# Optimization experiments

Measured on AMD Instinct MI355X. Metric: run time of the kernel, lower is better.

The kernel has to match this reference:

```python
import jax, jax.numpy as jnp
import numpy as np

B, S, D = 4, 2048, 1024
E = 8            # num_experts
H = 2 * D        # int(4*D*(1/top_k)) with top_k=2, scaling_factor='auto'


def setup_inputs() -> dict:
    key = jax.random.key(0)
    ks = jax.random.split(key, 8)
    sd = 1.0 / np.sqrt(D)
    sh = 1.0 / np.sqrt(H)
    return {
        "x": jax.random.normal(ks[0], (B, S, D), dtype=jnp.float32),
        "top_k": 2,
        "Wg": jax.random.uniform(ks[1], (D, E), jnp.float32, -sd, sd),
        "bg": jax.random.uniform(ks[2], (E,), jnp.float32, -sd, sd),
        "W1": jax.random.uniform(ks[3], (E, D, H), jnp.float32, -sd, sd),
        "b1": jax.random.uniform(ks[4], (E, H), jnp.float32, -sd, sd),
        "W2": jax.random.uniform(ks[5], (E, H, D), jnp.float32, -sh, sh),
        "b2": jax.random.uniform(ks[6], (E, D), jnp.float32, -sh, sh),
    }


def reference(x, top_k, Wg, bg, W1, b1, W2, b2):
    b, s, d = x.shape
    e = W1.shape[0]
    T = b * s
    xt = x.reshape(T, d)                                   # [T, D]
    gate_logits = xt @ Wg + bg                             # [T, E]
    gate_probas = jax.nn.softmax(gate_logits, axis=-1)
    topk_p, topk_i = jax.lax.top_k(gate_probas, top_k)     # [T, K]
    topk_p = topk_p / jnp.sum(topk_p, axis=-1, keepdims=True)
    # combine weights per expert: zero for unselected experts
    w = jnp.zeros((T, e), dtype=x.dtype).at[jnp.arange(T)[:, None], topk_i].add(topk_p)  # [T, E]
    # dense grouped FFN over experts; unselected experts are zero-weighted,
    # so the weighted combine matches the original gather-MLP-scatter math
    h = jax.nn.gelu(jnp.einsum('td,edh->teh', xt, W1) + b1, approximate=True)  # [T, E, H]
    y = jnp.einsum('teh,ehd->ted', h, W2) + b2             # [T, E, D]
    out = jnp.einsum('te,ted->td', w, y)                   # [T, D]
    return out.reshape(b, s, d)
```

## Files before the change

### kernel.cpp

```cpp
#include <hip/hip_runtime.h>

typedef unsigned short u16;
typedef short v8s __attribute__((ext_vector_type(8)));
typedef float v4f __attribute__((ext_vector_type(4)));
typedef u16 u16x8 __attribute__((ext_vector_type(8)));
typedef u16 u16x4 __attribute__((ext_vector_type(4)));

constexpr int Tn = 8192;
constexpr int Dd = 1024;
constexpr int Hh = 2048;
constexpr int Ee = 8;
constexpr int MAXP = 17;
constexpr int G1GEMM = 8 * 16 * MAXP;
constexpr int G1XTRA = 1024;

static __device__ __forceinline__ u16 f2bf(float v) {
  unsigned u = __float_as_uint(v);
  unsigned r = (u + 0x7fffu + ((u >> 16) & 1u)) >> 16;
  return (u16)r;
}

static __device__ __forceinline__ float bf2f(u16 v) {
  return __uint_as_float(((unsigned)v) << 16);
}

static __device__ __forceinline__ void gload_lds16(const u16* g, u16* l) {
  __builtin_amdgcn_global_load_lds(
      (const __attribute__((address_space(1))) unsigned int*)g,
      (__attribute__((address_space(3))) unsigned int*)l, 16, 0, 0);
}


static __device__ __forceinline__ void transpose_tile64(
    const float* __restrict__ ip, u16* __restrict__ op,
    int R, int C, int r0, int c0, bool permute, float (*tile)[65]) {
  int tid = threadIdx.x;
#pragma unroll
  for (int k = 0; k < 4; ++k) {
    int f = k * 256 + tid;
    int r = f >> 4, c4 = (f & 15) * 4;
    float4 v = *reinterpret_cast<const float4*>(ip + (size_t)(r0 + r) * C + c0 + c4);
    tile[r][c4] = v.x; tile[r][c4 + 1] = v.y; tile[r][c4 + 2] = v.z; tile[r][c4 + 3] = v.w;
  }
  __syncthreads();
  int j = tid & 7;
#pragma unroll
  for (int rr = 0; rr < 2; ++rr) {
    int oc = (tid >> 3) + rr * 32;
    u16x8 o;
    if (!permute) {
#pragma unroll
      for (int q = 0; q < 8; ++q) o[q] = f2bf(tile[j * 8 + q][oc]);
    } else {
#pragma unroll
      for (int q = 0; q < 8; ++q) {
        int p_ = j * 8 + q;
        int src = (p_ & 3) * 16 + (p_ >> 2);
        o[q] = f2bf(tile[src][oc]);
      }
    }
    *reinterpret_cast<u16x8*>(op + (size_t)(c0 + oc) * R + r0 + j * 8) = o;
  }
}

__global__ __launch_bounds__(256) void prep_kernel(
    const float* __restrict__ x, const float* __restrict__ Wg, const float* __restrict__ bg,
    int* __restrict__ topki, float* __restrict__ topkw, u16* __restrict__ xb,
    const float* __restrict__ W1, u16* __restrict__ w1t) {
  __shared__ float tile[64][65];
  int blk = blockIdx.x;

  if (blk < 4096) {
    int e = blk >> 9;
    int t = blk & 511;
    int cx = t & 31, cy = t >> 5;
    const float* ip = W1 + (size_t)e * Dd * Hh;
    u16* op = w1t + (size_t)e * Dd * Hh;
    transpose_tile64(ip, op, Dd, Hh, cy * 64, cx * 64, false, tile);
    return;
  }

  int lane = threadIdx.x & 63;
  int t = (blk - 4096) * 4 + (threadIdx.x >> 6);
  const float4* xr = reinterpret_cast<const float4*>(x + (size_t)t * Dd);
  float acc[8] = {0.f, 0.f, 0.f, 0.f, 0.f, 0.f, 0.f, 0.f};
#pragma unroll
  for (int it = 0; it < 4; ++it) {
    float4 xv = xr[it * 64 + lane];
    int r = it * 256 + lane * 4;
    ushort4 o;
    o.x = f2bf(xv.x); o.y = f2bf(xv.y); o.z = f2bf(xv.z); o.w = f2bf(xv.w);
    *reinterpret_cast<ushort4*>(xb + (size_t)t * Dd + r) = o;
    const float4* wr = reinterpret_cast<const float4*>(Wg + (size_t)r * 8);
    float xs[4] = {xv.x, xv.y, xv.z, xv.w};
#pragma unroll
    for (int q = 0; q < 4; ++q) {
      float4 a = wr[q * 2], b = wr[q * 2 + 1];
      acc[0] += xs[q] * a.x; acc[1] += xs[q] * a.y; acc[2] += xs[q] * a.z; acc[3] += xs[q] * a.w;
      acc[4] += xs[q] * b.x; acc[5] += xs[q] * b.y; acc[6] += xs[q] * b.z; acc[7] += xs[q] * b.w;
    }
  }
#pragma unroll
  for (int e = 0; e < 8; ++e) {
#pragma unroll
    for (int off = 32; off > 0; off >>= 1) acc[e] += __shfl_xor(acc[e], off, 64);
  }
  if (lane == 0) {
    float l[8];
    float mx = -1e30f;
#pragma unroll
    for (int e = 0; e < 8; ++e) { l[e] = acc[e] + bg[e]; mx = fmaxf(mx, l[e]); }
    int i0 = 0;
#pragma unroll
    for (int e = 1; e < 8; ++e) if (l[e] > l[i0]) i0 = e;
    int i1 = (i0 == 0) ? 1 : 0;
#pragma unroll
    for (int e = 0; e < 8; ++e) if (e != i0 && l[e] > l[i1]) i1 = e;
    float e0 = __expf(l[i0] - mx), e1 = __expf(l[i1] - mx);
    float inv = 1.0f / (e0 + e1);
    topki[2 * t] = i0; topki[2 * t + 1] = i1;
    topkw[2 * t] = e0 * inv; topkw[2 * t + 1] = e1 * inv;
  }
}

__global__ __launch_bounds__(512) void sort_kernel(
    const int* __restrict__ topki,
    int* __restrict__ offs, int* __restrict__ rows,
    int* __restrict__ panelE, int* __restrict__ panelB, int* __restrict__ nPanels) {
  __shared__ int scan[8][512];
  __shared__ int tot_l[8];
  __shared__ int offs_l[9];
  const int tt = threadIdx.x;
  const int base = tt * 32;

  int ev[32];
  int cnt[8] = {0, 0, 0, 0, 0, 0, 0, 0};
#pragma unroll
  for (int jj = 0; jj < 32; ++jj) {
    int e = topki[base + jj];
    ev[jj] = e;
#pragma unroll
    for (int q = 0; q < 8; ++q) cnt[q] += (e == q) ? 1 : 0;
  }
#pragma unroll
  for (int q = 0; q < 8; ++q) scan[q][tt] = cnt[q];
  __syncthreads();

  {
    int w = tt >> 6, l = tt & 63;
    int v[8];
    int s = 0;
#pragma unroll
    for (int jj = 0; jj < 8; ++jj) { v[jj] = scan[w][l * 8 + jj]; s += v[jj]; }
    int si = s;
#pragma unroll
    for (int off = 1; off < 64; off <<= 1) {
      int o = __shfl_up(si, off, 64);
      if (l >= off) si += o;
    }
    int run = si - s;
#pragma unroll
    for (int jj = 0; jj < 8; ++jj) { scan[w][l * 8 + jj] = run; run += v[jj]; }
    if (l == 63) tot_l[w] = si;
  }
  __syncthreads();

  if (tt == 0) {
    int o = 0;
#pragma unroll
    for (int e = 0; e < 8; ++e) { offs_l[e] = o; o += tot_l[e]; }
    offs_l[8] = o;
#pragma unroll
    for (int e = 0; e < 9; ++e) offs[e] = offs_l[e];
    int np = 0;
    for (int e = 0; e < 8; ++e) {
      for (int m0 = 0; m0 < tot_l[e]; m0 += 128) {
        panelE[np] = e;
        panelB[np] = offs_l[e] + m0;
        ++np;
      }
    }
    *nPanels = np;
  }
  __syncthreads();

#pragma unroll
  for (int jj = 0; jj < 32; ++jj) {
    int e = ev[jj];
    int idx = base + jj;
    int slot = scan[e][tt]++ + offs_l[e];
    rows[slot] = idx;
  }
}


__global__ __launch_bounds__(256, 2) void gemm1_kernel(
    const u16* __restrict__ xb, const u16* __restrict__ w1t, const float* __restrict__ b1,
    const int* __restrict__ offs, const int* __restrict__ rows,
    const int* __restrict__ panelE, const int* __restrict__ panelB,
    const int* __restrict__ nPanels, u16* __restrict__ hbuf,
    const float* __restrict__ W2, u16* __restrict__ w2t) {
  __shared__ __align__(16) u16 smem[2 * 128 * 64];
  u16* As = smem;
  u16* Bs = smem + 128 * 64;

  const int bid = blockIdx.x;
  if (bid >= G1GEMM) {
    float (*tile)[65] = reinterpret_cast<float (*)[65]>(smem);
    int tb = bid - G1GEMM;
#pragma unroll 1
    for (int s = 0; s < 4; ++s) {
      int tileid = tb * 4 + s;
      int e = tileid >> 9;
      int t = tileid & 511;
      int cx = t & 15, cy = t >> 4;
      if (s) __syncthreads();
      transpose_tile64(W2 + (size_t)e * Dd * Hh, w2t + (size_t)e * Dd * Hh,
                       Hh, Dd, cy * 64, cx * 64, true, tile);
    }
    return;
  }

  const int xcd = bid & 7;
  const int q = bid >> 3;
  const int n = q & 15;
  const int pi = (q >> 4) * 8 + xcd;
  if (pi >= *nPanels) return;
  const int e = panelE[pi];
  const int sbase = panelB[pi];
  const int lim = offs[e + 1];
  const int n0 = n * 128;

  const int tid = threadIdx.x;
  const int lane = tid & 63;
  const int wid = tid >> 6;
  const int wm = (wid >> 1) * 64;
  const int wn = (wid & 1) * 64;
  const int l16 = lane & 15;
  const int quad = lane >> 4;
  const int swz8 = (l16 & 7) * 8;

  const u16* aga[4];
  const u16* bga[4];
  u16* alds[4];
  u16* blds[4];
  const int lr = lane >> 3;
  const int g = (lane & 7) ^ (lr & 7);
  const int kcol = g * 8;
#pragma unroll
  for (int j = 0; j < 4; ++j) {
    int chunk = wid * 4 + j;
    int rowl = chunk * 8 + lr;
    int slot = sbase + rowl;
    if (slot >= lim) slot = sbase;
    aga[j] = xb + (size_t)(rows[slot] >> 1) * Dd + kcol;
    bga[j] = w1t + ((size_t)e * Hh + n0 + rowl) * Dd + kcol;
    alds[j] = As + chunk * 512;
    blds[j] = Bs + chunk * 512;
  }

  v4f acc[4][4];
#pragma unroll
  for (int i = 0; i < 4; ++i)
#pragma unroll
    for (int j = 0; j < 4; ++j) acc[i][j] = {0.f, 0.f, 0.f, 0.f};

  int rowAoff[4], rowBoff[4];
#pragma unroll
  for (int t_ = 0; t_ < 4; ++t_) {
    rowAoff[t_] = (wm + t_ * 16 + l16) * 64;
    rowBoff[t_] = (wn + t_ * 16 + l16) * 64;
  }

  for (int k0 = 0; k0 < Dd; k0 += 64) {
    __syncthreads();
#pragma unroll
    for (int j = 0; j < 4; ++j) gload_lds16(aga[j] + k0, alds[j]);
#pragma unroll
    for (int j = 0; j < 4; ++j) gload_lds16(bga[j] + k0, blds[j]);
    __syncthreads();

#pragma unroll
    for (int s = 0; s < 2; ++s) {
      int coff = ((s * 4 + quad) * 8) ^ swz8;
      v8s a[4], b[4];
#pragma unroll
      for (int mt = 0; mt < 4; ++mt)
        a[mt] = *reinterpret_cast<const v8s*>(&As[rowAoff[mt] + coff]);
#pragma unroll
      for (int nt = 0; nt < 4; ++nt)
        b[nt] = *reinterpret_cast<const v8s*>(&Bs[rowBoff[nt] + coff]);
#pragma unroll
      for (int mt = 0; mt < 4; ++mt)
#pragma unroll
        for (int nt = 0; nt < 4; ++nt)
          acc[mt][nt] = __builtin_amdgcn_mfma_f32_16x16x32_bf16(a[mt], b[nt], acc[mt][nt], 0, 0, 0);
    }
  }

  float b1v[4];
  const int ngbase = n0 + wn;
#pragma unroll
  for (int nt = 0; nt < 4; ++nt) b1v[nt] = b1[(size_t)e * Hh + ngbase + nt * 16 + l16];
#pragma unroll
  for (int mt = 0; mt < 4; ++mt) {
#pragma unroll
    for (int i = 0; i < 4; ++i) {
      int m = wm + mt * 16 + quad * 4 + i;
      if (sbase + m < lim) {
        u16x4 o;
#pragma unroll
        for (int nt = 0; nt < 4; ++nt) {
          float v = acc[mt][nt][i] + b1v[nt];
          float s = 1.0f / (1.0f + __expf(-1.5957691216057308f * (v + 0.044715f * v * v * v)));
          o[nt] = f2bf(v * s);
        }
        *reinterpret_cast<u16x4*>(hbuf + (size_t)(sbase + m) * Hh + ngbase + l16 * 4) = o;
      }
    }
  }
}

__global__ __launch_bounds__(256, 2) void gemm2_kernel(
    const u16* __restrict__ hbuf, const u16* __restrict__ w2t, const float* __restrict__ b2,
    const int* __restrict__ offs, const int* __restrict__ rows,
    const int* __restrict__ panelE, const int* __restrict__ panelB,
    const int* __restrict__ nPanels, u16* __restrict__ ybuf) {
  const int bid = blockIdx.x;
  const int xcd = bid & 7;
  const int q = bid >> 3;
  const int n = q & 7;
  const int pi = (q >> 3) * 8 + xcd;
  if (pi >= *nPanels) return;
  const int e = panelE[pi];
  const int sbase = panelB[pi];
  const int lim = offs[e + 1];
  const int n0 = n * 128;

  __shared__ __align__(16) u16 smem[2 * 128 * 64];
  u16* As = smem;
  u16* Bs = smem + 128 * 64;

  const int tid = threadIdx.x;
  const int lane = tid & 63;
  const int wid = tid >> 6;
  const int wm = (wid >> 1) * 64;
  const int wn = (wid & 1) * 64;
  const int l16 = lane & 15;
  const int quad = lane >> 4;
  const int swz8 = (l16 & 7) * 8;

  const u16* aga[4];
  const u16* bga[4];
  u16* alds[4];
  u16* blds[4];
  const int lr = lane >> 3;
  const int g = (lane & 7) ^ (lr & 7);
  const int kcol = g * 8;
#pragma unroll
  for (int j = 0; j < 4; ++j) {
    int chunk = wid * 4 + j;
    int rowl = chunk * 8 + lr;
    int slot = sbase + rowl;
    if (slot >= lim) slot = sbase;
    aga[j] = hbuf + (size_t)slot * Hh + kcol;
    bga[j] = w2t + ((size_t)e * Dd + n0 + rowl) * Hh + kcol;
    alds[j] = As + chunk * 512;
    blds[j] = Bs + chunk * 512;
  }

  v4f acc[4][4];
#pragma unroll
  for (int i = 0; i < 4; ++i)
#pragma unroll
    for (int j = 0; j < 4; ++j) acc[i][j] = {0.f, 0.f, 0.f, 0.f};

  int rowAoff[4], rowBoff[4];
#pragma unroll
  for (int t_ = 0; t_ < 4; ++t_) {
    rowAoff[t_] = (wm + t_ * 16 + l16) * 64;
    rowBoff[t_] = (wn + t_ * 16 + l16) * 64;
  }

  for (int k0 = 0; k0 < Hh; k0 += 64) {
    __syncthreads();
#pragma unroll
    for (int j = 0; j < 4; ++j) gload_lds16(aga[j] + k0, alds[j]);
#pragma unroll
    for (int j = 0; j < 4; ++j) gload_lds16(bga[j] + k0, blds[j]);
    __syncthreads();

#pragma unroll
    for (int s = 0; s < 2; ++s) {
      int coff = ((s * 4 + quad) * 8) ^ swz8;
      v8s a[4], b[4];
#pragma unroll
      for (int mt = 0; mt < 4; ++mt)
        a[mt] = *reinterpret_cast<const v8s*>(&As[rowAoff[mt] + coff]);
#pragma unroll
      for (int nt = 0; nt < 4; ++nt)
        b[nt] = *reinterpret_cast<const v8s*>(&Bs[rowBoff[nt] + coff]);
#pragma unroll
      for (int mt = 0; mt < 4; ++mt)
#pragma unroll
        for (int nt = 0; nt < 4; ++nt)
          acc[mt][nt] = __builtin_amdgcn_mfma_f32_16x16x32_bf16(a[mt], b[nt], acc[mt][nt], 0, 0, 0);
    }
  }

  float b2v[4];
  int ng[4];
#pragma unroll
  for (int nt = 0; nt < 4; ++nt) {
    ng[nt] = n0 + wn + nt * 16 + l16;
    b2v[nt] = b2[(size_t)e * Dd + ng[nt]];
  }
#pragma unroll
  for (int mt = 0; mt < 4; ++mt) {
#pragma unroll
    for (int i = 0; i < 4; ++i) {
      int m = wm + mt * 16 + quad * 4 + i;
      if (sbase + m < lim) {
        size_t rowbase = (size_t)rows[sbase + m] * Dd;
#pragma unroll
        for (int nt = 0; nt < 4; ++nt)
          ybuf[rowbase + ng[nt]] = f2bf(acc[mt][nt][i] + b2v[nt]);
      }
    }
  }
}

__global__ __launch_bounds__(256) void combine_kernel(
    const u16* __restrict__ ybuf, const float* __restrict__ topkw,
    float* __restrict__ out) {
  int idx = blockIdx.x * 256 + threadIdx.x;
  int t = idx >> 7;
  int d0 = (idx & 127) * 8;
  float w0 = topkw[2 * t], w1 = topkw[2 * t + 1];
  uint4 ya = *reinterpret_cast<const uint4*>(ybuf + (size_t)(2 * t) * Dd + d0);
  uint4 yb = *reinterpret_cast<const uint4*>(ybuf + (size_t)(2 * t + 1) * Dd + d0);
  float r[8];
  const unsigned* pa = &ya.x;
  const unsigned* pb = &yb.x;
#pragma unroll
  for (int j = 0; j < 4; ++j) {
    unsigned a = pa[j], b = pb[j];
    r[2 * j]     = w0 * bf2f((u16)(a & 0xffff)) + w1 * bf2f((u16)(b & 0xffff));
    r[2 * j + 1] = w0 * bf2f((u16)(a >> 16))    + w1 * bf2f((u16)(b >> 16));
  }
  float4* op = reinterpret_cast<float4*>(out + (size_t)t * Dd + d0);
  op[0] = make_float4(r[0], r[1], r[2], r[3]);
  op[1] = make_float4(r[4], r[5], r[6], r[7]);
}

extern "C" void kernel_launch(void* const* d_in, const int* in_sizes, int n_in,
                              void* d_out, int out_size, void* d_ws, size_t ws_size,
                              hipStream_t stream) {
  const float* x  = (const float*)d_in[0];
  const float* Wg = (const float*)d_in[2];
  const float* bg = (const float*)d_in[3];
  const float* W1 = (const float*)d_in[4];
  const float* b1 = (const float*)d_in[5];
  const float* W2 = (const float*)d_in[6];
  const float* b2 = (const float*)d_in[7];
  float* out = (float*)d_out;

  char* p = (char*)d_ws;
  auto take = [&](size_t bytes) {
    char* q = p;
    p += (bytes + 255) & ~(size_t)255;
    return q;
  };
  int*   offs       = (int*)take(64);
  int*   panelE     = (int*)take(1024);
  int*   panelB     = (int*)take(1024);
  int*   nPanels    = (int*)take(256);
  int*   topki      = (int*)take((size_t)Tn * 2 * sizeof(int));
  float* topkw      = (float*)take((size_t)Tn * 2 * sizeof(float));
  int*   rows       = (int*)take((size_t)Tn * 2 * sizeof(int));
  u16*   xb         = (u16*)take((size_t)Tn * Dd * 2);
  u16*   w1t        = (u16*)take((size_t)Ee * Dd * Hh * 2);
  u16*   w2t        = (u16*)take((size_t)Ee * Dd * Hh * 2);
  u16*   hbuf       = (u16*)take((size_t)Tn * 2 * Hh * 2);
  u16*   ybuf       = (u16*)take((size_t)Tn * 2 * Dd * 2);

  prep_kernel<<<6144, 256, 0, stream>>>(x, Wg, bg, topki, topkw, xb, W1, w1t);
  sort_kernel<<<1, 512, 0, stream>>>(topki, offs, rows, panelE, panelB, nPanels);
  gemm1_kernel<<<G1GEMM + G1XTRA, 256, 0, stream>>>(xb, w1t, b1, offs, rows,
                                                    panelE, panelB, nPanels, hbuf,
                                                    W2, w2t);
  gemm2_kernel<<<8 * 8 * MAXP, 256, 0, stream>>>(hbuf, w2t, b2, offs, rows,
                                                 panelE, panelB, nPanels, ybuf);
  combine_kernel<<<(Tn * Dd / 8) / 256, 256, 0, stream>>>(ybuf, topkw, out);
}
```

Baseline: 410.9 us.

## Fuse combine into gemm2 via atomic weighted adds, init output with bias in gemm1

Removes the separate combine kernel and the bf16 ybuf intermediate. Extra blocks appended to gemm1 initialise the output with the weighted sum of the b2 rows for each token's two experts. gemm2 then atomically adds the gate-weighted accumulator straight into the fp32 output. This saves one launch and a write and read of the intermediate, but adds two fp32 atomics per output element, whose contention and bandwidth cost may offset the savings, and it makes the summation order nondeterministic.

After: 429.6 us. 1.05x slower.

```diff
diff --git a/kernel.cpp b/kernel.cpp
--- a/kernel.cpp
+++ b/kernel.cpp
@@ -13,6 +13,7 @@
 constexpr int MAXP = 17;
 constexpr int G1GEMM = 8 * 16 * MAXP;
 constexpr int G1XTRA = 1024;
+constexpr int G1INIT = 512;
 
 static __device__ __forceinline__ u16 f2bf(float v) {
   unsigned u = __float_as_uint(v);
@@ -199,12 +200,33 @@
     const int* __restrict__ offs, const int* __restrict__ rows,
     const int* __restrict__ panelE, const int* __restrict__ panelB,
     const int* __restrict__ nPanels, u16* __restrict__ hbuf,
-    const float* __restrict__ W2, u16* __restrict__ w2t) {
+    const float* __restrict__ W2, u16* __restrict__ w2t,
+    const int* __restrict__ topki, const float* __restrict__ topkw,
+    const float* __restrict__ b2, float* __restrict__ out) {
   __shared__ __align__(16) u16 smem[2 * 128 * 64];
   u16* As = smem;
   u16* Bs = smem + 128 * 64;
 
   const int bid = blockIdx.x;
+  if (bid >= G1GEMM + G1XTRA) {
+    int rb = bid - (G1GEMM + G1XTRA);
+    int tid = threadIdx.x;
+#pragma unroll 1
+    for (int it = 0; it < 16; ++it) {
+      int c = it * (G1INIT * 256) + rb * 256 + tid;
+      int t = c >> 8;
+      int d0 = (c & 255) * 4;
+      float w0 = topkw[2 * t], w1 = topkw[2 * t + 1];
+      int e0 = topki[2 * t], e1 = topki[2 * t + 1];
+      float4 a = *reinterpret_cast<const float4*>(b2 + (size_t)e0 * Dd + d0);
+      float4 b = *reinterpret_cast<const float4*>(b2 + (size_t)e1 * Dd + d0);
+      float4 o;
+      o.x = w0 * a.x + w1 * b.x; o.y = w0 * a.y + w1 * b.y;
+      o.z = w0 * a.z + w1 * b.z; o.w = w0 * a.w + w1 * b.w;
+      *reinterpret_cast<float4*>(out + (size_t)t * Dd + d0) = o;
+    }
+    return;
+  }
   if (bid >= G1GEMM) {
     float (*tile)[65] = reinterpret_cast<float (*)[65]>(smem);
     int tb = bid - G1GEMM;
@@ -322,10 +344,11 @@
 }
 
 __global__ __launch_bounds__(256, 2) void gemm2_kernel(
-    const u16* __restrict__ hbuf, const u16* __restrict__ w2t, const float* __restrict__ b2,
+    const u16* __restrict__ hbuf, const u16* __restrict__ w2t,
     const int* __restrict__ offs, const int* __restrict__ rows,
+    const float* __restrict__ topkw,
     const int* __restrict__ panelE, const int* __restrict__ panelB,
-    const int* __restrict__ nPanels, u16* __restrict__ ybuf) {
+    const int* __restrict__ nPanels, float* __restrict__ out) {
   const int bid = blockIdx.x;
   const int xcd = bid & 7;
   const int q = bid >> 3;
@@ -408,49 +431,24 @@
     }
   }
 
-  float b2v[4];
   int ng[4];
 #pragma unroll
-  for (int nt = 0; nt < 4; ++nt) {
-    ng[nt] = n0 + wn + nt * 16 + l16;
-    b2v[nt] = b2[(size_t)e * Dd + ng[nt]];
-  }
+  for (int nt = 0; nt < 4; ++nt) ng[nt] = n0 + wn + nt * 16 + l16;
 #pragma unroll
   for (int mt = 0; mt < 4; ++mt) {
 #pragma unroll
     for (int i = 0; i < 4; ++i) {
       int m = wm + mt * 16 + quad * 4 + i;
       if (sbase + m < lim) {
-        size_t rowbase = (size_t)rows[sbase + m] * Dd;
+        int idx = rows[sbase + m];
+        float w = topkw[idx];
+        float* orow = out + (size_t)(idx >> 1) * Dd;
 #pragma unroll
         for (int nt = 0; nt < 4; ++nt)
-          ybuf[rowbase + ng[nt]] = f2bf(acc[mt][nt][i] + b2v[nt]);
+          atomicAdd(&orow[ng[nt]], w * acc[mt][nt][i]);
       }
     }
   }
-}
-
-__global__ __launch_bounds__(256) void combine_kernel(
-    const u16* __restrict__ ybuf, const float* __restrict__ topkw,
-    float* __restrict__ out) {
-  int idx = blockIdx.x * 256 + threadIdx.x;
-  int t = idx >> 7;
-  int d0 = (idx & 127) * 8;
-  float w0 = topkw[2 * t], w1 = topkw[2 * t + 1];
-  uint4 ya = *reinterpret_cast<const uint4*>(ybuf + (size_t)(2 * t) * Dd + d0);
-  uint4 yb = *reinterpret_cast<const uint4*>(ybuf + (size_t)(2 * t + 1) * Dd + d0);
-  float r[8];
-  const unsigned* pa = &ya.x;
-  const unsigned* pb = &yb.x;
-#pragma unroll
-  for (int j = 0; j < 4; ++j) {
-    unsigned a = pa[j], b = pb[j];
-    r[2 * j]     = w0 * bf2f((u16)(a & 0xffff)) + w1 * bf2f((u16)(b & 0xffff));
-    r[2 * j + 1] = w0 * bf2f((u16)(a >> 16))    + w1 * bf2f((u16)(b >> 16));
-  }
-  float4* op = reinterpret_cast<float4*>(out + (size_t)t * Dd + d0);
-  op[0] = make_float4(r[0], r[1], r[2], r[3]);
-  op[1] = make_float4(r[4], r[5], r[6], r[7]);
 }
 
 extern "C" void kernel_launch(void* const* d_in, const int* in_sizes, int n_in,
@@ -482,14 +480,12 @@
   u16*   w1t        = (u16*)take((size_t)Ee * Dd * Hh * 2);
   u16*   w2t        = (u16*)take((size_t)Ee * Dd * Hh * 2);
   u16*   hbuf       = (u16*)take((size_t)Tn * 2 * Hh * 2);
-  u16*   ybuf       = (u16*)take((size_t)Tn * 2 * Dd * 2);
 
   prep_kernel<<<6144, 256, 0, stream>>>(x, Wg, bg, topki, topkw, xb, W1, w1t);
   sort_kernel<<<1, 512, 0, stream>>>(topki, offs, rows, panelE, panelB, nPanels);
-  gemm1_kernel<<<G1GEMM + G1XTRA, 256, 0, stream>>>(xb, w1t, b1, offs, rows,
-                                                    panelE, panelB, nPanels, hbuf,
-                                                    W2, w2t);
-  gemm2_kernel<<<8 * 8 * MAXP, 256, 0, stream>>>(hbuf, w2t, b2, offs, rows,
-                                                 panelE, panelB, nPanels, ybuf);
-  combine_kernel<<<(Tn * Dd / 8) / 256, 256, 0, stream>>>(ybuf, topkw, out);
-}
+  gemm1_kernel<<<G1GEMM + G1XTRA + G1INIT, 256, 0, stream>>>(
+      xb, w1t, b1, offs, rows, panelE, panelB, nPanels, hbuf,
+      W2, w2t, topki, topkw, b2, out);
+  gemm2_kernel<<<8 * 8 * MAXP, 256, 0, stream>>>(hbuf, w2t, offs, rows, topkw,
+                                                 panelE, panelB, nPanels, out);
+}
```
